# Performance work log

Measured on AMD Instinct MI355X. Metric: run time of the kernel, lower is better.

Reference implementation:

```python
import jax, jax.numpy as jnp
from jax import lax
import numpy as np

B, NG, NC = 4, 513, 512  # batch, grid size N, coef size N-1

_STENCILS = [[[-1/6, 2/3], [-1/3, -1/6]],
             [[2/3, -1/6], [-1/6, -1/3]],
             [[-1/6, -1/3], [2/3, -1/6]],
             [[-1/3, -1/6], [-1/6, 2/3]]]

def _kernel():
    # torch: vstack 4 (1,1,2,2) kernels -> permute(1,0,2,3) => (out=1, in=4, 2, 2)
    return jnp.asarray(_STENCILS, jnp.float32)[None]

def darcy(x, a, kernel):
    # x: (B,1,N,N), a: (B,1,N-1,N-1)
    N = x.shape[-1]
    X = jnp.concatenate([x[:, :, 1:N, :N-1] * a,
                         x[:, :, 1:N, 1:] * a,
                         x[:, :, :N-1, 1:] * a,
                         x[:, :, :N-1, :N-1] * a], axis=1)  # (B,4,N-1,N-1)
    Ax = lax.conv_general_dilated(X, kernel, (1, 1), 'VALID')  # (B,1,N-2,N-2)
    return jnp.pad(Ax, ((0, 0), (0, 0), (1, 1), (1, 1)))

def _conv3(x, w):
    # x: (Cin,H,W), w: (Cout,Cin,3,3), padding=1
    return lax.conv_general_dilated(x[None], w, (1, 1), ((1, 1), (1, 1)))[0]
_CONVB = jax.vmap(_conv3)

def mcc(x, w):
    # per-sample complex 3x3 conv == torch multi_channel_conv diagonal trick
    yr = _CONVB(x.real, w.real) - _CONVB(x.imag, w.imag)
    yi = _CONVB(x.real, w.imag) + _CONVB(x.imag, w.real)
    return yr + 1j * yi

def conjT(w):
    # transpose(-4,-3).transpose(-2,-1).conj()
    return jnp.conj(jnp.swapaxes(jnp.swapaxes(w, 1, 2), -2, -1))

def expand(r):
    Bb, C, M, N = r.shape
    Z = jnp.zeros((Bb, C, 2 * (M + 1), 2 * (N + 1)), r.dtype)
    Z = Z.at[:, :, 1:M+1, 1:N+1].set(r)
    Z = Z.at[:, :, M+2:, 1:N+1].set(-r[:, :, ::-1, :])
    Z = Z.at[:, :, 1:M+1, N+2:].set(-r[:, :, :, ::-1])
    Z = Z.at[:, :, M+2:, N+2:].set(r[:, :, ::-1, ::-1])
    kg = jnp.arange(-M - 1, N + 1, dtype=jnp.float32) * jnp.float32(np.pi)
    ik2 = 1.0 / (kg[:, None] ** 2 + kg[None, :] ** 2)
    ik2 = ik2.at[M + 1, N + 1].set(1.0)
    N2 = 2 * (N + 1)
    lo = N2 // 2 - N2 // 4
    hi = N2 // 2 + N2 // 4 + 1
    return Z, ik2[lo:hi, lo:hi][None, None]

def H_apply(r, w1, w2, w3, wt):
    N1 = r.shape[-1]
    rsym, ik2 = expand(r)
    N2 = rsym.shape[-1]
    lo = N2 // 2 - N2 // 4
    hi = N2 // 2 + N2 // 4 + 1
    rh = jnp.fft.fftshift(jnp.fft.ifft2(rsym, axes=(2, 3)), axes=(2, 3))[:, :, lo:hi, lo:hi]
    for w in (w1, w2, w3):
        rh = mcc(rh, w)
    out = rh * wt * ik2
    for w in (conjT(w3), conjT(w2), conjT(w1)):
        out = mcc(out, w)
    pl = N2 // 4 + 1
    pr = N2 - N2 // 2 - pl
    out = jnp.pad(out, ((0, 0), (0, 0), (pl, pr), (pl, pr)))
    e = jnp.fft.fft2(jnp.fft.ifftshift(out, axes=(2, 3)), axes=(2, 3)).real
    return e[:, :, :N1, :N1]

def fns_step(x, f, a, dinv, kernel, ws):
    # Jacobi smoother, w=3/4, M=10
    for _ in range(10):
        r = f - darcy(x, a, kernel)
        x = x.at[:, :, 1:-1, 1:-1].add(0.75 * dinv * r[:, :, 1:-1, 1:-1])
    r = f - darcy(x, a, kernel)
    e = H_apply(r[:, :, 1:-1, 1:-1], *ws)
    e = jnp.pad(e, ((0, 0), (0, 0), (1, 1), (1, 1)))
    Ae = darcy(e, a, kernel)
    alpha = (jnp.sum(r * e, axis=(1, 2, 3)) / jnp.sum(Ae * e, axis=(1, 2, 3)))[:, None, None, None]
    return x + alpha * e

def _forward(f, coef, w1, w2, w3, wt, K):
    kernel = _kernel()
    diag_k = (2.0 / 3.0) * jnp.ones((1, 1, 2, 2), jnp.float32)
    dinv = 1.0 / lax.conv_general_dilated(coef, diag_k, (1, 1), 'VALID')
    ws = (w1, w2, w3, wt)
    x = jnp.zeros_like(f)
    for _ in range(K):
        x = fns_step(x, f, coef, dinv, kernel, ws)
    r = f - darcy(x, coef, kernel)
    return jnp.linalg.norm(r.reshape(-1)) / jnp.linalg.norm(f.reshape(-1))

def setup_inputs():
    key = jax.random.key(0)
    ks = jax.random.split(key, 12)
    s = jnp.float32(0.1)
    inp = {
        'f': jax.random.normal(ks[0], (B, 1, NG, NG), jnp.float32),
        'coef': jax.random.uniform(ks[1], (B, 1, NC, NC), jnp.float32) + 0.1,
        'u': jnp.zeros((B, 1, NG, NG), jnp.float32),
        'w1r': jax.random.normal(ks[2], (B, 4, 1, 3, 3), jnp.float32) * s,
        'w1i': jax.random.normal(ks[3], (B, 4, 1, 3, 3), jnp.float32) * s,
        'w2r': jax.random.normal(ks[4], (B, 4, 4, 3, 3), jnp.float32) * s,
        'w2i': jax.random.normal(ks[5], (B, 4, 4, 3, 3), jnp.float32) * s,
        'w3r': jax.random.normal(ks[6], (B, 1, 4, 3, 3), jnp.float32) * s,
        'w3i': jax.random.normal(ks[7], (B, 1, 4, 3, 3), jnp.float32) * s,
        'wtr': jax.random.normal(ks[8], (B, 1, NG, NG), jnp.float32) * s,
        'wti': jax.random.normal(ks[9], (B, 1, NG, NG), jnp.float32) * s,
        'epoch': 101,
    }
    return inp

def reference(f, coef, u, w1r, w1i, w2r, w2i, w3r, w3i, wtr, wti, epoch):
    K = (epoch - 1) // 100 + 1
    w1 = w1r + 1j * w1i
    w2 = w2r + 1j * w2i
    w3 = w3r + 1j * w3i
    wt = wtr + 1j * wti
    return _forward(f, coef, w1, w2, w3, wt, K)
```

## Files before the change

### kernel.cpp

```cpp
#include <hip/hip_runtime.h>
#include <math.h>

#ifndef M_PI
#define M_PI 3.14159265358979323846
#endif

#define NGRID 513
#define NCELL 512
#define NINT  511
#define NB    4

constexpr int N2G = NGRID * NGRID;
constexpr int NI2 = NINT * NINT;
constexpr int NQ  = 257 * 257;

typedef unsigned short ushort;
typedef unsigned int uint32;
typedef __attribute__((ext_vector_type(8))) short short8;
typedef __attribute__((ext_vector_type(8))) unsigned short ushort8;
typedef __attribute__((ext_vector_type(4))) float f32x4;

__device__ __forceinline__ ushort f2bf(float x) {
    unsigned u = __float_as_uint(x);
    unsigned r = u + 0x7FFFu + ((u >> 16) & 1u);
    return (ushort)(r >> 16);
}
__device__ __forceinline__ float bf2f(ushort h) {
    return __uint_as_float(((unsigned)h) << 16);
}

__device__ __forceinline__ float rhq_read(const float* __restrict__ rq,
                                          int i, int j) {
    float s = 1.0f;
    if (i > 256) { i = 512 - i; s = -s; }
    if (j > 256) { j = 512 - j; s = -s; }
    return s * rq[i * 257 + j];
}

__device__ __forceinline__ float2 scale_wt(float x0, float x1, float wr, float wi,
                                           int gr, int gc) {
    int du = gr - 256, dv = gc - 256;
    float ik2;
    if (du == 0 && dv == 0)
        ik2 = 1.0f;
    else
        ik2 = (float)(1.0 / (9.869604401089358 * (double)(du * du + dv * dv)));
    return make_float2((x0 * wr - x1 * wi) * ik2, (x0 * wi + x1 * wr) * ik2);
}

__device__ __forceinline__ float darcyA(const float* __restrict__ x,
                                        const float* __restrict__ a,
                                        int i, int j) {
    const float c23 = 2.0f / 3.0f, c16 = 1.0f / 6.0f, c13 = 1.0f / 3.0f;
    float a00 = a[(i - 1) * NCELL + (j - 1)];
    float a01 = a[(i - 1) * NCELL + j];
    float a10 = a[i * NCELL + (j - 1)];
    float a11 = a[i * NCELL + j];
    const float* xm = x + (i - 1) * NGRID;
    const float* xc = x + i * NGRID;
    const float* xp = x + (i + 1) * NGRID;
    return c23 * (a00 + a01 + a10 + a11) * xc[j]
         - c16 * ((a00 + a01) * xm[j] + (a10 + a11) * xp[j]
                + (a00 + a10) * xc[j - 1] + (a01 + a11) * xc[j + 1])
         - c13 * (a00 * xm[j - 1] + a01 * xm[j + 1]
                + a10 * xp[j - 1] + a11 * xp[j + 1]);
}

__global__ void k_stencil(const float* __restrict__ xin,
                          const float* __restrict__ a,
                          const float* __restrict__ f,
                          float* __restrict__ out, int mode,
                          ushort* __restrict__ tBh, ushort* __restrict__ tBl) {
    __shared__ float st[16][17];
    int b = blockIdx.z;
    int j = blockIdx.x * 16 + threadIdx.x;
    int i = blockIdx.y * 16 + threadIdx.y;
    const float* xb = xin + (long long)b * N2G;
    const float* ab = a + (long long)b * NCELL * NCELL;
    bool ingrid = (i < NGRID && j < NGRID);
    bool interior = ingrid && i >= 1 && i <= NINT && j >= 1 && j <= NINT;
    float v = 0.0f;
    long long idx = (long long)b * N2G + (long long)i * NGRID + j;
    if (interior) {
        float Ax = darcyA(xb, ab, i, j);
        v = (mode == 0) ? f[idx] - Ax : Ax;
    } else if (ingrid) {
        v = (mode == 0) ? f[idx] : 0.0f;
    }
    if (ingrid) out[idx] = v;
    if (mode == 0 && tBh) {
        st[threadIdx.y][threadIdx.x] = v;
        __syncthreads();
        int tx = threadIdx.x, ty = threadIdx.y;
        int i2 = blockIdx.y * 16 + tx;
        int j2 = blockIdx.x * 16 + ty;
        if (i2 >= 1 && i2 <= NINT && j2 >= 1 && j2 <= NINT) {
            float rv = st[tx][ty];
            ushort h = f2bf(rv);
            long long o = (long long)b * 511 * 512
                        + (long long)(j2 - 1) * 512 + (i2 - 1);
            tBh[o] = h;
            tBl[o] = f2bf(rv - bf2f(h));
        }
    }
}

__global__ void k_jacobi5(const float* __restrict__ xin,
                          const float* __restrict__ a,
                          const float* __restrict__ f,
                          const float* __restrict__ dinv,
                          float* __restrict__ out) {
    __shared__ float sx[26][26];
    __shared__ float sa[25][26];
    __shared__ float sf[24][24];
    __shared__ float sd[24][24];
    __shared__ float sp[2][24][26];
    const float c23 = 2.0f / 3.0f, c16 = 1.0f / 6.0f, c13 = 1.0f / 3.0f;
    int b = blockIdx.z;
    const float* xb = xin + (long long)b * N2G;
    const float* ab = a + (long long)b * NCELL * NCELL;
    const float* fb = f + (long long)b * N2G;
    const float* db = dinv + (long long)b * NI2;
    int ox = blockIdx.x * 16, oy = blockIdx.y * 16;
    int tx = threadIdx.x, ty = threadIdx.y;
    int tid = ty * 16 + tx;

    for (int idx = tid; idx < 26 * 26; idx += 256) {
        int ly = idx / 26, lx = idx % 26;
        int gy = oy - 5 + ly, gx = ox - 5 + lx;
        bool in = (gy >= 0 && gy < NGRID && gx >= 0 && gx < NGRID);
        sx[ly][lx] = in ? xb[(long long)gy * NGRID + gx] : 0.0f;
    }
    for (int idx = tid; idx < 25 * 25; idx += 256) {
        int ly = idx / 25, lx = idx % 25;
        int gy = oy - 5 + ly, gx = ox - 5 + lx;
        bool in = (gy >= 0 && gy < NCELL && gx >= 0 && gx < NCELL);
        sa[ly][lx] = in ? ab[(long long)gy * NCELL + gx] : 0.0f;
    }
    for (int idx = tid; idx < 24 * 24; idx += 256) {
        int ly = idx / 24, lx = idx % 24;
        int gy = oy - 4 + ly, gx = ox - 4 + lx;
        bool ing = (gy >= 0 && gy < NGRID && gx >= 0 && gx < NGRID);
        bool itr = (gy >= 1 && gy <= NINT && gx >= 1 && gx <= NINT);
        sf[ly][lx] = ing ? fb[(long long)gy * NGRID + gx] : 0.0f;
        sd[ly][lx] = itr ? db[(long long)(gy - 1) * NINT + (gx - 1)] : 0.0f;
    }
    __syncthreads();

    for (int idx = tid; idx < 24 * 24; idx += 256) {
        int ly = idx / 24, lx = idx % 24;
        int gy = oy - 4 + ly, gx = ox - 4 + lx;
        float v = 0.0f;
        if (gy >= 0 && gy < NGRID && gx >= 0 && gx < NGRID) {
            float xc = sx[ly + 1][lx + 1];
            if (gy >= 1 && gy <= NINT && gx >= 1 && gx <= NINT) {
                float a00 = sa[ly][lx], a01 = sa[ly][lx + 1];
                float a10 = sa[ly + 1][lx], a11 = sa[ly + 1][lx + 1];
                float Ax = c23 * (a00 + a01 + a10 + a11) * xc
                    - c16 * ((a00 + a01) * sx[ly][lx + 1] + (a10 + a11) * sx[ly + 2][lx + 1]
                           + (a00 + a10) * sx[ly + 1][lx] + (a01 + a11) * sx[ly + 1][lx + 2])
                    - c13 * (a00 * sx[ly][lx] + a01 * sx[ly][lx + 2]
                           + a10 * sx[ly + 2][lx] + a11 * sx[ly + 2][lx + 2]);
                v = xc + 0.75f * sd[ly][lx] * (sf[ly][lx] - Ax);
            } else {
                v = xc;
            }
        }
        sp[0][ly][lx] = v;
    }
    __syncthreads();

    #pragma unroll 1
    for (int s = 2; s <= 4; ++s) {
        int sz = 24 - 2 * (s - 1);
        int cur = (s - 1) & 1, prv = s & 1;
        for (int idx = tid; idx < sz * sz; idx += 256) {
            int ly = idx / sz, lx = idx % sz;
            int gy = oy - (5 - s) + ly, gx = ox - (5 - s) + lx;
            float v = 0.0f;
            if (gy >= 0 && gy < NGRID && gx >= 0 && gx < NGRID) {
                float xc = sp[prv][ly + 1][lx + 1];
                if (gy >= 1 && gy <= NINT && gx >= 1 && gx <= NINT) {
                    int ar = ly + s - 1, ac = lx + s - 1;
                    float a00 = sa[ar][ac], a01 = sa[ar][ac + 1];
                    float a10 = sa[ar + 1][ac], a11 = sa[ar + 1][ac + 1];
                    float Ax = c23 * (a00 + a01 + a10 + a11) * xc
                        - c16 * ((a00 + a01) * sp[prv][ly][lx + 1] + (a10 + a11) * sp[prv][ly + 2][lx + 1]
                               + (a00 + a10) * sp[prv][ly + 1][lx] + (a01 + a11) * sp[prv][ly + 1][lx + 2])
                        - c13 * (a00 * sp[prv][ly][lx] + a01 * sp[prv][ly][lx + 2]
                               + a10 * sp[prv][ly + 2][lx] + a11 * sp[prv][ly + 2][lx + 2]);
                    int fr = ly + s - 1, fc = lx + s - 1;
                    v = xc + 0.75f * sd[fr][fc] * (sf[fr][fc] - Ax);
                } else {
                    v = xc;
                }
            }
            sp[cur][ly][lx] = v;
        }
        __syncthreads();
    }

    {
        int gy = oy + ty, gx = ox + tx;
        if (gy < NGRID && gx < NGRID) {
            float v;
            float xc = sp[1][ty + 1][tx + 1];
            if (gy >= 1 && gy <= NINT && gx >= 1 && gx <= NINT) {
                int ar = ty + 4, ac = tx + 4;
                float a00 = sa[ar][ac], a01 = sa[ar][ac + 1];
                float a10 = sa[ar + 1][ac], a11 = sa[ar + 1][ac + 1];
                float Ax = c23 * (a00 + a01 + a10 + a11) * xc
                    - c16 * ((a00 + a01) * sp[1][ty][tx + 1] + (a10 + a11) * sp[1][ty + 2][tx + 1]
                           + (a00 + a10) * sp[1][ty + 1][tx] + (a01 + a11) * sp[1][ty + 1][tx + 2])
                    - c13 * (a00 * sp[1][ty][tx] + a01 * sp[1][ty][tx + 2]
                           + a10 * sp[1][ty + 2][tx] + a11 * sp[1][ty + 2][tx + 2]);
                v = xc + 0.75f * sd[ty + 4][tx + 4] * (sf[ty + 4][tx + 4] - Ax);
            } else {
                v = xc;
            }
            out[(long long)b * N2G + (long long)gy * NGRID + gx] = v;
        }
    }
}

__global__ void k_dinv(const float* __restrict__ a, float* __restrict__ dinv) {
    long long idx = (long long)blockIdx.x * blockDim.x + threadIdx.x;
    if (idx >= (long long)NB * NI2) return;
    int b = (int)(idx / NI2);
    int rem = (int)(idx % NI2);
    int p = rem / NINT, q = rem % NINT;
    const float* ab = a + (long long)b * NCELL * NCELL;
    float s = ab[p * NCELL + q] + ab[p * NCELL + q + 1]
            + ab[(p + 1) * NCELL + q] + ab[(p + 1) * NCELL + q + 1];
    dinv[idx] = 1.0f / ((2.0f / 3.0f) * s);
}

__device__ __forceinline__ void wsplit(double v, ushort* Dh, ushort* Dl, int idx) {
    float vf = (float)v;
    ushort h = f2bf(vf);
    Dh[idx] = h;
    Dl[idx] = f2bf(vf - bf2f(h));
}

__global__ void k_genDSTA(ushort* __restrict__ Dh, ushort* __restrict__ Dl) {
    int idx = blockIdx.x * 256 + threadIdx.x;
    if (idx >= 513 * 512) return;
    int u = idx / 512, k = idx % 512;
    double v = 0.0;
    if (k < 511) {
        int t = ((u - 256) * (k + 1)) % 1024;
        if (t < 0) t += 1024;
        v = sin((M_PI / 512.0) * (double)t);
    }
    wsplit(v, Dh, Dl, idx);
}

__global__ void k_genDSTB(ushort* __restrict__ Dh, ushort* __restrict__ Dl) {
    int idx = blockIdx.x * 256 + threadIdx.x;
    if (idx >= 513 * 512) return;
    int v = idx / 512, k = idx % 512;
    double val = 0.0;
    if (k < 511) {
        int t = ((v - 256) * (k + 1)) % 1024;
        if (t < 0) t += 1024;
        val = sin((M_PI / 512.0) * (double)t) * (-1.0 / 262144.0);
    }
    wsplit(val, Dh, Dl, idx);
}

__global__ void k_genFA(ushort* __restrict__ Dh, ushort* __restrict__ Dl) {
    int idx = blockIdx.x * 256 + threadIdx.x;
    if (idx >= 511 * 1056) return;
    int y = idx / 1056, k = idx % 1056;
    double v = 0.0;
    if (k < 1026) {
        int m = (k < 513) ? k : (k - 513);
        long t = ((long)y * (m - 255)) % 1025;
        if (t < 0) t += 1025;
        double ang = (2.0 * M_PI / 1025.0) * (double)t;
        v = (k < 513) ? cos(ang) : -sin(ang);
    }
    wsplit(v, Dh, Dl, idx);
}

__global__ void k_genFB(ushort* __restrict__ Dh, ushort* __restrict__ Dl) {
    int idx = blockIdx.x * 256 + threadIdx.x;
    if (idx >= 1022 * 1056) return;
    int n = idx / 1056, k = idx % 1056;
    double v = 0.0;
    if (k < 1026) {
        int m = (k < 513) ? k : (k - 513);
        int y = (n < 511) ? n : (n - 511);
        long t = ((long)y * (m - 255)) % 1025;
        if (t < 0) t += 1025;
        double ang = (2.0 * M_PI / 1025.0) * (double)t;
        bool ktop = (k < 513), nleft = (n < 511);
        if (ktop && nleft)        v = cos(ang);
        else if (ktop && !nleft)  v = -sin(ang);
        else if (!ktop && nleft)  v = sin(ang);
        else                      v = cos(ang);
    }
    wsplit(v, Dh, Dl, idx);
}

__global__ void k_redA(const float* __restrict__ P, int nsplit, int Mr,
                       ushort* __restrict__ Dh, ushort* __restrict__ Dl) {
    int b = blockIdx.y;
    int idx = blockIdx.x * 256 + threadIdx.x;
    if (idx >= Mr * 512) return;
    int m = idx / 512, k = idx % 512;
    float v = 0.0f;
    if (k < 511) {
        long long base = (long long)m * 511 + k;
        long long str = (long long)Mr * 511;
        #pragma unroll 4
        for (int s = 0; s < nsplit; ++s)
            v += P[((long long)b * nsplit + s) * str + base];
    }
    long long o = (long long)b * Mr * 512 + idx;
    ushort h = f2bf(v);
    Dh[o] = h;
    Dl[o] = f2bf(v - bf2f(h));
}

__global__ void k_redBt(const float* __restrict__ P, int nsplit,
                        ushort* __restrict__ Dh, ushort* __restrict__ Dl) {
    int b = blockIdx.y;
    int idx = blockIdx.x * 256 + threadIdx.x;
    if (idx >= 511 * 1056) return;
    int n = idx / 1056, k = idx % 1056;
    float v = 0.0f;
    if (k < 1026) {
        int row = (k < 513) ? n : (511 + n);
        int col = (k < 513) ? k : (k - 513);
        long long base = (long long)row * 513 + col;
        float acc = 0.0f;
        #pragma unroll 4
        for (int s = 0; s < nsplit; ++s)
            acc += P[((long long)b * nsplit + s) * (1022LL * 513) + base];
        v = (k < 513) ? acc : -acc;
    }
    long long o = (long long)b * 511 * 1056 + idx;
    ushort h = f2bf(v);
    Dh[o] = h;
    Dl[o] = f2bf(v - bf2f(h));
}

__global__ __launch_bounds__(256) void k_mgemm(
    const ushort* __restrict__ Ah, const ushort* __restrict__ Al, long long bsA,
    const ushort* __restrict__ Bh, const ushort* __restrict__ Bl, long long bsB,
    float* __restrict__ C, long long bsC,
    int M, int N, int Kp, int nsplit) {
    __shared__ ushort sAh[128 * 40];
    __shared__ ushort sAl[128 * 40];
    __shared__ ushort sBh[128 * 40];
    __shared__ ushort sBl[128 * 40];

    int bz = blockIdx.z, b = bz / nsplit, ks = bz % nsplit;
    int kchunk = (((Kp + nsplit - 1) / nsplit) + 31) & ~31;
    int kbeg = ks * kchunk;
    int kend = min(Kp, kbeg + kchunk);

    Ah += b * bsA; Al += b * bsA;
    Bh += b * bsB; Bl += b * bsB;
    C += ((long long)b * nsplit + ks) * bsC;

    int bm = blockIdx.y * 128, bn = blockIdx.x * 128;
    int tid = threadIdx.x;
    int wave = tid >> 6, lane = tid & 63;
    int wm = (wave >> 1) * 64, wn = (wave & 1) * 64;
    int quad = lane >> 4, l16 = lane & 15;

    f32x4 zf = {0.f, 0.f, 0.f, 0.f};
    f32x4 acc[4][4];
    #pragma unroll
    for (int i = 0; i < 4; ++i)
        #pragma unroll
        for (int j = 0; j < 4; ++j) acc[i][j] = zf;

    int srow = tid >> 2;
    int sk8 = (tid & 3) * 8;

    for (int kt = kbeg; kt < kend; kt += 32) {
        #pragma unroll
        for (int h = 0; h < 2; ++h) {
            int row = srow + 64 * h;
            ushort8 vh = {0, 0, 0, 0, 0, 0, 0, 0};
            ushort8 vl = {0, 0, 0, 0, 0, 0, 0, 0};
            int gm = bm + row;
            if (gm < M) {
                vh = *(const ushort8*)(Ah + (long long)gm * Kp + kt + sk8);
                vl = *(const ushort8*)(Al + (long long)gm * Kp + kt + sk8);
            }
            *(ushort8*)(sAh + row * 40 + sk8) = vh;
            *(ushort8*)(sAl + row * 40 + sk8) = vl;
            ushort8 wh = {0, 0, 0, 0, 0, 0, 0, 0};
            ushort8 wl = {0, 0, 0, 0, 0, 0, 0, 0};
            int gn = bn + row;
            if (gn < N) {
                wh = *(const ushort8*)(Bh + (long long)gn * Kp + kt + sk8);
                wl = *(const ushort8*)(Bl + (long long)gn * Kp + kt + sk8);
            }
            *(ushort8*)(sBh + row * 40 + sk8) = wh;
            *(ushort8*)(sBl + row * 40 + sk8) = wl;
        }
        __syncthreads();

        short8 afh[4], afl[4], bfh[4], bfl[4];
        #pragma unroll
        for (int t = 0; t < 4; ++t) {
            int ar = wm + t * 16 + l16;
            afh[t] = *(const short8*)(sAh + ar * 40 + quad * 8);
            afl[t] = *(const short8*)(sAl + ar * 40 + quad * 8);
            int br = wn + t * 16 + l16;
            bfh[t] = *(const short8*)(sBh + br * 40 + quad * 8);
            bfl[t] = *(const short8*)(sBl + br * 40 + quad * 8);
        }
        #pragma unroll
        for (int mt = 0; mt < 4; ++mt)
            #pragma unroll
            for (int nt = 0; nt < 4; ++nt) {
                acc[mt][nt] = __builtin_amdgcn_mfma_f32_16x16x32_bf16(
                    afh[mt], bfh[nt], acc[mt][nt], 0, 0, 0);
                acc[mt][nt] = __builtin_amdgcn_mfma_f32_16x16x32_bf16(
                    afh[mt], bfl[nt], acc[mt][nt], 0, 0, 0);
                acc[mt][nt] = __builtin_amdgcn_mfma_f32_16x16x32_bf16(
                    afl[mt], bfh[nt], acc[mt][nt], 0, 0, 0);
            }
        __syncthreads();
    }

    #pragma unroll
    for (int mt = 0; mt < 4; ++mt) {
        #pragma unroll
        for (int r = 0; r < 4; ++r) {
            int gm = bm + wm + mt * 16 + quad * 4 + r;
            if (gm >= M) continue;
            long long rowoff = (long long)gm * N;
            #pragma unroll
            for (int nt = 0; nt < 4; ++nt) {
                int gn = bn + wn + nt * 16 + l16;
                if (gn < N) C[rowoff + gn] = acc[mt][nt][r];
            }
        }
    }
}

__global__ void k_reduce(const float* __restrict__ Pr,
                         float* __restrict__ outR,
                         int MN, int N, int ldo, long long bsOut, int nsplit) {
    int b = blockIdx.y;
    for (int idx = blockIdx.x * 256 + threadIdx.x; idx < MN;
         idx += gridDim.x * 256) {
        float sr = 0.0f;
        #pragma unroll 4
        for (int s = 0; s < nsplit; ++s)
            sr += Pr[((long long)b * nsplit + s) * MN + idx];
        int m = idx / N, n = idx - m * N;
        outR[(long long)b * bsOut + (long long)m * ldo + n] = sr;
    }
}

__device__ __forceinline__ float2 cmul(float2 a, float2 b) {
    return make_float2(a.x * b.x - a.y * b.y, a.x * b.y + a.y * b.x);
}

__global__ void k_compose(const float* __restrict__ w1r, const float* __restrict__ w1i,
                          const float* __restrict__ w2r, const float* __restrict__ w2i,
                          const float* __restrict__ w3r, const float* __restrict__ w3i,
                          float* __restrict__ kc) {
    int chain = blockIdx.x, b = blockIdx.y;
    int tid = threadIdx.x;
    __shared__ float2 sW1[4][9], sW2[16][9], sW3[4][9], sW21[4][25];
    for (int idx = tid; idx < 36; idx += 128) {
        int c = idx / 9, s = idx % 9, p = s / 3, q = s % 3;
        if (chain == 0) {
            int i1 = b * 36 + c * 9 + p * 3 + q;
            sW1[c][s] = make_float2(w1r[i1], w1i[i1]);
            sW3[c][s] = make_float2(w3r[i1], w3i[i1]);
        } else {
            int it = b * 36 + c * 9 + q * 3 + p;
            sW1[c][s] = make_float2(w3r[it], -w3i[it]);
            sW3[c][s] = make_float2(w1r[it], -w1i[it]);
        }
    }
    for (int idx = tid; idx < 144; idx += 128) {
        int co = idx / 36, r = idx % 36, ci = r / 9, s = r % 9, p = s / 3, q = s % 3;
        int iw = (chain == 0) ? (b * 144 + co * 36 + ci * 9 + p * 3 + q)
                              : (b * 144 + ci * 36 + co * 9 + q * 3 + p);
        float iv = w2i[iw];
        sW2[co * 4 + ci][s] = make_float2(w2r[iw], (chain == 0) ? iv : -iv);
    }
    __syncthreads();
    for (int idx = tid; idx < 100; idx += 128) {
        int cm = idx / 25, r = idx % 25, di = r / 5 - 2, dj = r % 5 - 2;
        float2 acc = make_float2(0.f, 0.f);
        for (int c1 = 0; c1 < 4; ++c1)
            for (int p = 0; p < 3; ++p)
                for (int q = 0; q < 3; ++q) {
                    int ei = di - (p - 1) + 1, ej = dj - (q - 1) + 1;
                    if (ei >= 0 && ei < 3 && ej >= 0 && ej < 3) {
                        float2 t = cmul(sW2[cm * 4 + c1][p * 3 + q], sW1[c1][ei * 3 + ej]);
                        acc.x += t.x; acc.y += t.y;
                    }
                }
        sW21[cm][r] = acc;
    }
    __syncthreads();
    for (int idx = tid; idx < 49; idx += 128) {
        int di = idx / 7 - 3, dj = idx % 7 - 3;
        float2 acc = make_float2(0.f, 0.f);
        for (int cm = 0; cm < 4; ++cm)
            for (int p = 0; p < 3; ++p)
                for (int q = 0; q < 3; ++q) {
                    int ei = di - (p - 1), ej = dj - (q - 1);
                    if (ei >= -2 && ei <= 2 && ej >= -2 && ej <= 2) {
                        float2 t = cmul(sW3[cm][p * 3 + q], sW21[cm][(ei + 2) * 5 + (ej + 2)]);
                        acc.x += t.x; acc.y += t.y;
                    }
                }
        ((float2*)kc)[(b * 2 + chain) * 49 + idx] = acc;
    }
}

template <int MODE>
__global__ __launch_bounds__(256) void k_conv7(
    const float* __restrict__ xr, const float* __restrict__ xi,
    const float* __restrict__ wtr, const float* __restrict__ wti,
    const float* __restrict__ kc,
    float* __restrict__ outr, float* __restrict__ outi,
    ushort* __restrict__ oAh, ushort* __restrict__ oAl) {
    constexpr bool CPLX = (MODE == 1);
    __shared__ float2 tile[38][23];
    __shared__ float2 kt[49];
    int b = blockIdx.z;
    int tid = threadIdx.y * 16 + threadIdx.x;
    const float2* kb = (const float2*)kc + (b * 2 + MODE) * 49;
    for (int idx = tid; idx < 49; idx += 256) kt[idx] = kb[idx];
    int row_base = blockIdx.y * 32 - 3;
    int col_base = blockIdx.x * 16 - 3;
    const float* rq = xr + (long long)b * NQ;
    for (int idx = tid; idx < 38 * 22; idx += 256) {
        int r = idx / 22, c = idx % 22;
        int gr = row_base + r, gc = col_base + c;
        float vr = 0.0f, vi = 0.0f;
        if (gr >= 0 && gr < NGRID && gc >= 0 && gc < NGRID) {
            if (MODE == 0) {
                vr = rhq_read(rq, gr, gc);
            } else {
                long long g = (long long)b * N2G + (long long)gr * NGRID + gc;
                float2 sc = scale_wt(xr[g], xi[g], wtr[g], wti[g], gr, gc);
                vr = sc.x; vi = sc.y;
            }
        }
        tile[r][c] = make_float2(vr, vi);
    }
    __syncthreads();

    int tx = threadIdx.x, r0 = threadIdx.y * 2;
    float2 acc[2];
    acc[0] = make_float2(0.f, 0.f);
    acc[1] = make_float2(0.f, 0.f);
    #pragma unroll
    for (int t = 0; t < 7; ++t) {
        float2 kv[7];
        #pragma unroll
        for (int s = 0; s < 7; ++s) kv[s] = kt[s * 7 + t];
        #pragma unroll
        for (int rr = 0; rr < 8; ++rr) {
            float2 xv = tile[r0 + rr][tx + t];
            #pragma unroll
            for (int s = 0; s < 7; ++s) {
                int orow = rr - s;
                if (orow >= 0 && orow < 2) {
                    acc[orow].x += kv[s].x * xv.x;
                    acc[orow].y += kv[s].y * xv.x;
                    if (CPLX) {
                        acc[orow].x -= kv[s].y * xv.y;
                        acc[orow].y += kv[s].x * xv.y;
                    }
                }
            }
        }
    }
    int gc = blockIdx.x * 16 + tx;
    if (gc >= NGRID) return;
    #pragma unroll
    for (int r = 0; r < 2; ++r) {
        int gr = blockIdx.y * 32 + r0 + r;
        if (gr < NGRID) {
            if (MODE == 0) {
                long long g = (long long)b * N2G + (long long)gr * NGRID + gc;
                outr[g] = acc[r].x;
                outi[g] = acc[r].y;
            } else {
                long long o = (long long)b * 513 * 1056
                            + (long long)gr * 1056 + gc;
                ushort h = f2bf(acc[r].x);
                oAh[o] = h;
                oAl[o] = f2bf(acc[r].x - bf2f(h));
                ushort h2 = f2bf(acc[r].y);
                oAh[o + 513] = h2;
                oAl[o + 513] = f2bf(acc[r].y - bf2f(h2));
            }
        }
    }
}

template <int CHAIN>
__global__ __launch_bounds__(256) void k_ring7(
    const float* __restrict__ xr, const float* __restrict__ xi,
    const float* __restrict__ wtr, const float* __restrict__ wti,
    const float* __restrict__ w1r, const float* __restrict__ w1i,
    const float* __restrict__ w2r, const float* __restrict__ w2i,
    const float* __restrict__ w3r, const float* __restrict__ w3i,
    float* __restrict__ outr, float* __restrict__ outi,
    ushort* __restrict__ oAh, ushort* __restrict__ oAl) {
    constexpr bool CPLX = (CHAIN == 1);
    __shared__ float2 W1s[4][9], W2s[16][9], W3s[4][9];
    __shared__ float2 Y[4][4][68];
    __shared__ float2 Z[4][3][66];
    int side = blockIdx.y, b = blockIdx.z;
    int u0 = blockIdx.x * 64;
    int ulo = (side < 2) ? 0 : 2;
    int uhi = (side < 2) ? (NGRID - 1) : (NGRID - 3);
    if (u0 > uhi) return;
    int tid = threadIdx.x;
    const float* rq = xr + (long long)b * NQ;

    for (int idx = tid; idx < 36; idx += 256) {
        int c = idx / 9, s = idx % 9, p = s / 3, q = s % 3;
        if (CHAIN == 0) {
            int i1 = b * 36 + c * 9 + p * 3 + q;
            W1s[c][s] = make_float2(w1r[i1], w1i[i1]);
            W3s[c][s] = make_float2(w3r[i1], w3i[i1]);
        } else {
            int it = b * 36 + c * 9 + q * 3 + p;
            W1s[c][s] = make_float2(w3r[it], -w3i[it]);
            W3s[c][s] = make_float2(w1r[it], -w1i[it]);
        }
    }
    for (int idx = tid; idx < 144; idx += 256) {
        int co = idx / 36, r = idx % 36, ci = r / 9, s = r % 9, p = s / 3, q = s % 3;
        int iw = (CHAIN == 0) ? (b * 144 + co * 36 + ci * 9 + p * 3 + q)
                              : (b * 144 + ci * 36 + co * 9 + q * 3 + p);
        float iv = w2i[iw];
        W2s[co * 4 + ci][s] = make_float2(w2r[iw], (CHAIN == 0) ? iv : -iv);
    }
    __syncthreads();

    for (int idx = tid; idx < 4 * 4 * 68; idx += 256) {
        int ch = idx / (4 * 68), r = idx % (4 * 68), d = r / 68, uu = r % 68;
        int u = u0 - 2 + uu;
        float2 acc = make_float2(0.f, 0.f);
        if (u >= 0 && u < NGRID) {
            int i, j;
            if (side == 0)      { i = d;       j = u; }
            else if (side == 1) { i = 512 - d; j = u; }
            else if (side == 2) { i = u;       j = d; }
            else                { i = u;       j = 512 - d; }
            for (int p = 0; p < 3; ++p)
                for (int q = 0; q < 3; ++q) {
                    int ii = i + p - 1, jj = j + q - 1;
                    if (ii >= 0 && ii < NGRID && jj >= 0 && jj < NGRID) {
                        float vr, vi;
                        if (CHAIN == 0) {
                            vr = rhq_read(rq, ii, jj);
                            vi = 0.0f;
                        } else {
                            long long g = (long long)b * N2G
                                        + (long long)ii * NGRID + jj;
                            float2 sc = scale_wt(xr[g], xi[g], wtr[g], wti[g],
                                                 ii, jj);
                            vr = sc.x; vi = sc.y;
                        }
                        float2 w = W1s[ch][p * 3 + q];
                        acc.x += w.x * vr - w.y * vi;
                        acc.y += w.x * vi + w.y * vr;
                    }
                }
        }
        Y[ch][d][uu] = acc;
    }
    __syncthreads();

    for (int idx = tid; idx < 4 * 3 * 66; idx += 256) {
        int co = idx / (3 * 66), r = idx % (3 * 66), d = r / 66, uu = r % 66;
        int u = u0 - 1 + uu;
        float2 acc = make_float2(0.f, 0.f);
        if (u >= 0 && u < NGRID) {
            for (int p = 0; p < 3; ++p)
                for (int q = 0; q < 3; ++q) {
                    int dd, du;
                    if (side == 0)      { dd = p - 1; du = q - 1; }
                    else if (side == 1) { dd = 1 - p; du = q - 1; }
                    else if (side == 2) { dd = q - 1; du = p - 1; }
                    else                { dd = 1 - q; du = p - 1; }
                    int d2 = d + dd, uy = uu + 1 + du;
                    if (d2 >= 0) {
                        for (int ci = 0; ci < 4; ++ci) {
                            float2 yv = Y[ci][d2][uy];
                            float2 w = W2s[co * 4 + ci][p * 3 + q];
                            acc.x += w.x * yv.x - w.y * yv.y;
                            acc.y += w.x * yv.y + w.y * yv.x;
                        }
                    }
                }
        }
        Z[co][d][uu] = acc;
    }
    __syncthreads();

    for (int idx = tid; idx < 128; idx += 256) {
        int d = idx / 64, uu = idx % 64;
        int u = u0 + uu;
        if (u < ulo || u > uhi) continue;
        float2 acc = make_float2(0.f, 0.f);
        for (int p = 0; p < 3; ++p)
            for (int q = 0; q < 3; ++q) {
                int dd, du;
                if (side == 0)      { dd = p - 1; du = q - 1; }
                else if (side == 1) { dd = 1 - p; du = q - 1; }
                else if (side == 2) { dd = q - 1; du = p - 1; }
                else                { dd = 1 - q; du = p - 1; }
                int d2 = d + dd, uz = uu + 1 + du;
                if (d2 >= 0) {
                    for (int ci = 0; ci < 4; ++ci) {
                        float2 zv = Z[ci][d2][uz];
                        float2 w = W3s[ci][p * 3 + q];
                        acc.x += w.x * zv.x - w.y * zv.y;
                        acc.y += w.x * zv.y + w.y * zv.x;
                    }
                }
            }
        int i, j;
        if (side == 0)      { i = d;       j = u; }
        else if (side == 1) { i = 512 - d; j = u; }
        else if (side == 2) { i = u;       j = d; }
        else                { i = u;       j = 512 - d; }
        if (CHAIN == 0) {
            long long g = (long long)b * N2G + (long long)i * NGRID + j;
            outr[g] = acc.x;
            outi[g] = acc.y;
        } else {
            long long o = (long long)b * 513 * 1056 + (long long)i * 1056 + j;
            ushort h = f2bf(acc.x);
            oAh[o] = h;
            oAl[o] = f2bf(acc.x - bf2f(h));
            ushort h2 = f2bf(acc.y);
            oAh[o + 513] = h2;
            oAl[o + 513] = f2bf(acc.y - bf2f(h2));
        }
    }
}

__global__ void k_dot2(const float* __restrict__ r, const float* __restrict__ e,
                       const float* __restrict__ Ae, float* __restrict__ red) {
    int b = blockIdx.y;
    const float* rb = r + (long long)b * N2G;
    const float* eb = e + (long long)b * N2G;
    const float* ab = Ae + (long long)b * N2G;
    float s1 = 0.0f, s2 = 0.0f;
    for (int i = blockIdx.x * blockDim.x + threadIdx.x; i < N2G;
         i += gridDim.x * blockDim.x) {
        float ev = eb[i];
        s1 += rb[i] * ev;
        s2 += ab[i] * ev;
    }
    #pragma unroll
    for (int o = 32; o > 0; o >>= 1) {
        s1 += __shfl_down(s1, o);
        s2 += __shfl_down(s2, o);
    }
    __shared__ float l1[4], l2[4];
    int wid = threadIdx.x >> 6;
    if ((threadIdx.x & 63) == 0) { l1[wid] = s1; l2[wid] = s2; }
    __syncthreads();
    if (threadIdx.x == 0) {
        atomicAdd(&red[2 * b], l1[0] + l1[1] + l1[2] + l1[3]);
        atomicAdd(&red[2 * b + 1], l2[0] + l2[1] + l2[2] + l2[3]);
    }
}

__global__ void k_update(float* __restrict__ x, const float* __restrict__ e,
                         const float* __restrict__ red) {
    long long idx = (long long)blockIdx.x * blockDim.x + threadIdx.x;
    if (idx >= (long long)NB * N2G) return;
    int b = (int)(idx / N2G);
    float alpha = red[2 * b] / red[2 * b + 1];
    x[idx] += alpha * e[idx];
}

__global__ void k_norm(const float* __restrict__ r, const float* __restrict__ f,
                       float* __restrict__ red) {
    float s1 = 0.0f, s2 = 0.0f;
    for (long long i = (long long)blockIdx.x * blockDim.x + threadIdx.x;
         i < (long long)NB * N2G; i += (long long)gridDim.x * blockDim.x) {
        float rv = r[i], fv = f[i];
        s1 += rv * rv;
        s2 += fv * fv;
    }
    #pragma unroll
    for (int o = 32; o > 0; o >>= 1) {
        s1 += __shfl_down(s1, o);
        s2 += __shfl_down(s2, o);
    }
    __shared__ float l1[4], l2[4];
    int wid = threadIdx.x >> 6;
    if ((threadIdx.x & 63) == 0) { l1[wid] = s1; l2[wid] = s2; }
    __syncthreads();
    if (threadIdx.x == 0) {
        atomicAdd(&red[8], l1[0] + l1[1] + l1[2] + l1[3]);
        atomicAdd(&red[9], l2[0] + l2[1] + l2[2] + l2[3]);
    }
}

__global__ void k_final(const float* __restrict__ red, float* __restrict__ out) {
    out[0] = sqrtf(red[8] / red[9]);
}

extern "C" void kernel_launch(void* const* d_in, const int* in_sizes, int n_in,
                              void* d_out, int out_size, void* d_ws, size_t ws_size,
                              hipStream_t stream) {
    (void)in_sizes; (void)n_in; (void)out_size; (void)ws_size;
    const float* f    = (const float*)d_in[0];
    const float* coef = (const float*)d_in[1];
    const float* w1r  = (const float*)d_in[3];
    const float* w1i  = (const float*)d_in[4];
    const float* w2r  = (const float*)d_in[5];
    const float* w2i  = (const float*)d_in[6];
    const float* w3r  = (const float*)d_in[7];
    const float* w3i  = (const float*)d_in[8];
    const float* wtr  = (const float*)d_in[9];
    const float* wti  = (const float*)d_in[10];
    float* out = (float*)d_out;

    float* ws = (float*)d_ws;
    size_t off = 0;
    auto alloc = [&](long long n) {
        float* p = ws + off;
        off += (size_t)((n + 3) & ~3LL);
        return p;
    };
    float* x0   = alloc((long long)NB * N2G);
    float* x1   = alloc((long long)NB * N2G);
    float* rr   = alloc((long long)NB * N2G);
    float* ee   = alloc((long long)NB * N2G);
    float* dinv = alloc((long long)NB * NI2);
    float* c1r  = alloc((long long)NB * 4 * N2G);
    float* c1i  = alloc((long long)NB * 4 * N2G);
    float* c2r  = alloc((long long)NB * 4 * N2G);
    float* c2i  = alloc((long long)NB * 4 * N2G);
    float* pr   = c1r;
    float* or_  = alloc((long long)NB * N2G);
    float* oi_  = alloc((long long)NB * N2G);
    float* rhq  = alloc((long long)NB * NQ);
    float* red  = alloc(16);
    ushort* sGh  = (ushort*)alloc(513 * 512 / 2);
    ushort* sGl  = (ushort*)alloc(513 * 512 / 2);
    ushort* sGth = (ushort*)alloc(513 * 512 / 2);
    ushort* sGtl = (ushort*)alloc(513 * 512 / 2);
    ushort* sFAh = (ushort*)alloc(511 * 1056 / 2);
    ushort* sFAl = (ushort*)alloc(511 * 1056 / 2);
    ushort* sFBh = (ushort*)alloc(1022 * 1056 / 2);
    ushort* sFBl = (ushort*)alloc(1022 * 1056 / 2);
    ushort* dA2h = (ushort*)alloc((long long)NB * 257 * 512 / 2);
    ushort* dA2l = (ushort*)alloc((long long)NB * 257 * 512 / 2);
    ushort* dA3h = (ushort*)alloc((long long)NB * 513 * 1056 / 2);
    ushort* dA3l = (ushort*)alloc((long long)NB * 513 * 1056 / 2);
    ushort* dB1h = (ushort*)alloc((long long)NB * 511 * 512 / 2);
    ushort* dB1l = (ushort*)alloc((long long)NB * 511 * 512 / 2);
    ushort* dB4h = (ushort*)alloc((long long)NB * 511 * 1056 / 2);
    ushort* dB4l = (ushort*)alloc((long long)NB * 511 * 1056 / 2);
    float* kcomp = alloc(NB * 2 * 49 * 2);
    float* Ae   = or_;

    dim3 blk2(16, 16);
    dim3 grdS(33, 33, NB);
    dim3 grdC(33, 17, NB);
    dim3 grdR(9, 4, NB);
    const int SP = 4;

    hipMemsetAsync(x0, 0, (size_t)NB * N2G * sizeof(float), stream);
    hipMemsetAsync(dA3h, 0, (size_t)NB * 513 * 1056 * 2 * 2, stream);
    hipMemsetAsync(dB1h, 0, (size_t)NB * 511 * 512 * 2 * 2, stream);
    k_dinv<<<dim3((NB * NI2 + 255) / 256), dim3(256), 0, stream>>>(coef, dinv);
    k_genDSTA<<<dim3((513 * 512 + 255) / 256), dim3(256), 0, stream>>>(sGh, sGl);
    k_genDSTB<<<dim3((513 * 512 + 255) / 256), dim3(256), 0, stream>>>(sGth, sGtl);
    k_genFA<<<dim3((511 * 1056 + 255) / 256), dim3(256), 0, stream>>>(sFAh, sFAl);
    k_genFB<<<dim3((1022 * 1056 + 255) / 256), dim3(256), 0, stream>>>(sFBh, sFBl);
    k_compose<<<dim3(2, NB), dim3(128), 0, stream>>>(w1r, w1i, w2r, w2i, w3r, w3i, kcomp);

    float* xa = x0;
    float* xb = x1;
    for (int step = 0; step < 2; ++step) {
        for (int it = 0; it < 2; ++it) {
            k_jacobi5<<<grdS, blk2, 0, stream>>>(xa, coef, f, dinv, xb);
            float* t = xa; xa = xb; xb = t;
        }
        k_stencil<<<grdS, blk2, 0, stream>>>(xa, coef, f, rr, 0, dB1h, dB1l);

        k_mgemm<<<dim3(4, 3, NB * SP), dim3(256), 0, stream>>>(
            sGh, sGl, 0, dB1h, dB1l, (long long)511 * 512,
            pr, (long long)257 * 511, 257, 511, 512, SP);
        k_redA<<<dim3((257 * 512 + 255) / 256, NB), dim3(256), 0, stream>>>(
            pr, SP, 257, dA2h, dA2l);
        k_mgemm<<<dim3(3, 3, NB * SP), dim3(256), 0, stream>>>(
            dA2h, dA2l, (long long)257 * 512, sGth, sGtl, 0,
            pr, (long long)NQ, 257, 257, 512, SP);
        k_reduce<<<dim3(259, NB), dim3(256), 0, stream>>>(
            pr, rhq, NQ, 257, 257, (long long)NQ, SP);

        k_conv7<0><<<grdC, blk2, 0, stream>>>(
            rhq, nullptr, nullptr, nullptr, kcomp, or_, oi_, nullptr, nullptr);
        k_ring7<0><<<grdR, dim3(256), 0, stream>>>(
            rhq, nullptr, nullptr, nullptr,
            w1r, w1i, w2r, w2i, w3r, w3i, or_, oi_, nullptr, nullptr);
        k_conv7<1><<<grdC, blk2, 0, stream>>>(
            or_, oi_, wtr, wti, kcomp, nullptr, nullptr, dA3h, dA3l);
        k_ring7<1><<<grdR, dim3(256), 0, stream>>>(
            or_, oi_, wtr, wti,
            w1r, w1i, w2r, w2i, w3r, w3i, nullptr, nullptr, dA3h, dA3l);

        k_mgemm<<<dim3(5, 8, NB * 4), dim3(256), 0, stream>>>(
            sFBh, sFBl, 0, dA3h, dA3l, (long long)513 * 1056,
            pr, 1022LL * 513, 1022, 513, 1056, 4);
        k_redBt<<<dim3(2109, NB), dim3(256), 0, stream>>>(pr, 4, dB4h, dB4l);
        k_mgemm<<<dim3(4, 4, NB * SP), dim3(256), 0, stream>>>(
            sFAh, sFAl, 0, dB4h, dB4l, (long long)511 * 1056,
            pr, (long long)NI2, 511, 511, 1056, SP);
        hipMemsetAsync(ee, 0, (size_t)NB * N2G * sizeof(float), stream);
        k_reduce<<<dim3(1024, NB), dim3(256), 0, stream>>>(
            pr, ee + NGRID + 1, NI2, NINT, NGRID, (long long)N2G, SP);

        k_stencil<<<grdS, blk2, 0, stream>>>(ee, coef, nullptr, Ae, 2,
                                             nullptr, nullptr);
        hipMemsetAsync(red, 0, 8 * sizeof(float), stream);
        k_dot2<<<dim3(64, NB), dim3(256), 0, stream>>>(rr, ee, Ae, red);
        k_update<<<dim3((NB * N2G + 255) / 256), dim3(256), 0, stream>>>(xa, ee, red);
    }
    k_stencil<<<grdS, blk2, 0, stream>>>(xa, coef, f, rr, 0, nullptr, nullptr);
    hipMemsetAsync(red + 8, 0, 2 * sizeof(float), stream);
    k_norm<<<dim3(256), dim3(256), 0, stream>>>(rr, f, red);
    k_final<<<dim3(1), dim3(1), 0, stream>>>(red, out);
}
```

Before: 683.1 us.

## Fuse Jacobi smoothing with residual, Ae into dot, and final update into norm

```diff
diff --git a/kernel.cpp b/kernel.cpp
--- a/kernel.cpp
+++ b/kernel.cpp
@@ -66,55 +66,22 @@
                 + a10 * xp[j - 1] + a11 * xp[j + 1]);
 }
 
-__global__ void k_stencil(const float* __restrict__ xin,
-                          const float* __restrict__ a,
-                          const float* __restrict__ f,
-                          float* __restrict__ out, int mode,
-                          ushort* __restrict__ tBh, ushort* __restrict__ tBl) {
+template <int RES>
+__global__ __launch_bounds__(256) void k_jacobi5R(
+    const float* __restrict__ xin, const float* __restrict__ a,
+    const float* __restrict__ f, const float* __restrict__ dinv,
+    float* __restrict__ out, float* __restrict__ rout,
+    ushort* __restrict__ tBh, ushort* __restrict__ tBl) {
+    constexpr int H  = RES ? 6 : 5;
+    constexpr int SX = 16 + 2 * H;
+    constexpr int SA = SX - 1;
+    constexpr int SF = 16 + 2 * (H - 1);
+    __shared__ float sx[SX][SX];
+    __shared__ float sa[SA][SA + 1];
+    __shared__ float sf[SF][SF];
+    __shared__ float sd[SF][SF];
+    __shared__ float sp[2][SF][SF + 2];
     __shared__ float st[16][17];
-    int b = blockIdx.z;
-    int j = blockIdx.x * 16 + threadIdx.x;
-    int i = blockIdx.y * 16 + threadIdx.y;
-    const float* xb = xin + (long long)b * N2G;
-    const float* ab = a + (long long)b * NCELL * NCELL;
-    bool ingrid = (i < NGRID && j < NGRID);
-    bool interior = ingrid && i >= 1 && i <= NINT && j >= 1 && j <= NINT;
-    float v = 0.0f;
-    long long idx = (long long)b * N2G + (long long)i * NGRID + j;
-    if (interior) {
-        float Ax = darcyA(xb, ab, i, j);
-        v = (mode == 0) ? f[idx] - Ax : Ax;
-    } else if (ingrid) {
-        v = (mode == 0) ? f[idx] : 0.0f;
-    }
-    if (ingrid) out[idx] = v;
-    if (mode == 0 && tBh) {
-        st[threadIdx.y][threadIdx.x] = v;
-        __syncthreads();
-        int tx = threadIdx.x, ty = threadIdx.y;
-        int i2 = blockIdx.y * 16 + tx;
-        int j2 = blockIdx.x * 16 + ty;
-        if (i2 >= 1 && i2 <= NINT && j2 >= 1 && j2 <= NINT) {
-            float rv = st[tx][ty];
-            ushort h = f2bf(rv);
-            long long o = (long long)b * 511 * 512
-                        + (long long)(j2 - 1) * 512 + (i2 - 1);
-            tBh[o] = h;
-            tBl[o] = f2bf(rv - bf2f(h));
-        }
-    }
-}
-
-__global__ void k_jacobi5(const float* __restrict__ xin,
-                          const float* __restrict__ a,
-                          const float* __restrict__ f,
-                          const float* __restrict__ dinv,
-                          float* __restrict__ out) {
-    __shared__ float sx[26][26];
-    __shared__ float sa[25][26];
-    __shared__ float sf[24][24];
-    __shared__ float sd[24][24];
-    __shared__ float sp[2][24][26];
     const float c23 = 2.0f / 3.0f, c16 = 1.0f / 6.0f, c13 = 1.0f / 3.0f;
     int b = blockIdx.z;
     const float* xb = xin + (long long)b * N2G;
@@ -125,21 +92,21 @@
     int tx = threadIdx.x, ty = threadIdx.y;
     int tid = ty * 16 + tx;
 
-    for (int idx = tid; idx < 26 * 26; idx += 256) {
-        int ly = idx / 26, lx = idx % 26;
-        int gy = oy - 5 + ly, gx = ox - 5 + lx;
+    for (int idx = tid; idx < SX * SX; idx += 256) {
+        int ly = idx / SX, lx = idx % SX;
+        int gy = oy - H + ly, gx = ox - H + lx;
         bool in = (gy >= 0 && gy < NGRID && gx >= 0 && gx < NGRID);
         sx[ly][lx] = in ? xb[(long long)gy * NGRID + gx] : 0.0f;
     }
-    for (int idx = tid; idx < 25 * 25; idx += 256) {
-        int ly = idx / 25, lx = idx % 25;
-        int gy = oy - 5 + ly, gx = ox - 5 + lx;
+    for (int idx = tid; idx < SA * SA; idx += 256) {
+        int ly = idx / SA, lx = idx % SA;
+        int gy = oy - H + ly, gx = ox - H + lx;
         bool in = (gy >= 0 && gy < NCELL && gx >= 0 && gx < NCELL);
         sa[ly][lx] = in ? ab[(long long)gy * NCELL + gx] : 0.0f;
     }
-    for (int idx = tid; idx < 24 * 24; idx += 256) {
-        int ly = idx / 24, lx = idx % 24;
-        int gy = oy - 4 + ly, gx = ox - 4 + lx;
+    for (int idx = tid; idx < SF * SF; idx += 256) {
+        int ly = idx / SF, lx = idx % SF;
+        int gy = oy - (H - 1) + ly, gx = ox - (H - 1) + lx;
         bool ing = (gy >= 0 && gy < NGRID && gx >= 0 && gx < NGRID);
         bool itr = (gy >= 1 && gy <= NINT && gx >= 1 && gx <= NINT);
         sf[ly][lx] = ing ? fb[(long long)gy * NGRID + gx] : 0.0f;
@@ -147,9 +114,9 @@
     }
     __syncthreads();
 
-    for (int idx = tid; idx < 24 * 24; idx += 256) {
-        int ly = idx / 24, lx = idx % 24;
-        int gy = oy - 4 + ly, gx = ox - 4 + lx;
+    for (int idx = tid; idx < SF * SF; idx += 256) {
+        int ly = idx / SF, lx = idx % SF;
+        int gy = oy - (H - 1) + ly, gx = ox - (H - 1) + lx;
         float v = 0.0f;
         if (gy >= 0 && gy < NGRID && gx >= 0 && gx < NGRID) {
             float xc = sx[ly + 1][lx + 1];
@@ -171,12 +138,12 @@
     __syncthreads();
 
     #pragma unroll 1
-    for (int s = 2; s <= 4; ++s) {
-        int sz = 24 - 2 * (s - 1);
+    for (int s = 2; s <= 5; ++s) {
+        int sz = 16 + 2 * (H - s);
         int cur = (s - 1) & 1, prv = s & 1;
         for (int idx = tid; idx < sz * sz; idx += 256) {
             int ly = idx / sz, lx = idx % sz;
-            int gy = oy - (5 - s) + ly, gx = ox - (5 - s) + lx;
+            int gy = oy - (H - s) + ly, gx = ox - (H - s) + lx;
             float v = 0.0f;
             if (gy >= 0 && gy < NGRID && gx >= 0 && gx < NGRID) {
                 float xc = sp[prv][ly + 1][lx + 1];
@@ -200,25 +167,40 @@
         __syncthreads();
     }
 
-    {
-        int gy = oy + ty, gx = ox + tx;
+    int gy = oy + ty, gx = ox + tx;
+    long long gidx = (long long)b * N2G + (long long)gy * NGRID + gx;
+    if constexpr (!RES) {
+        if (gy < NGRID && gx < NGRID) out[gidx] = sp[0][ty][tx];
+    } else {
+        float rv = 0.0f;
         if (gy < NGRID && gx < NGRID) {
-            float v;
-            float xc = sp[1][ty + 1][tx + 1];
+            float x5 = sp[0][ty + 1][tx + 1];
+            out[gidx] = x5;
             if (gy >= 1 && gy <= NINT && gx >= 1 && gx <= NINT) {
-                int ar = ty + 4, ac = tx + 4;
-                float a00 = sa[ar][ac], a01 = sa[ar][ac + 1];
-                float a10 = sa[ar + 1][ac], a11 = sa[ar + 1][ac + 1];
-                float Ax = c23 * (a00 + a01 + a10 + a11) * xc
-                    - c16 * ((a00 + a01) * sp[1][ty][tx + 1] + (a10 + a11) * sp[1][ty + 2][tx + 1]
-                           + (a00 + a10) * sp[1][ty + 1][tx] + (a01 + a11) * sp[1][ty + 1][tx + 2])
-                    - c13 * (a00 * sp[1][ty][tx] + a01 * sp[1][ty][tx + 2]
-                           + a10 * sp[1][ty + 2][tx] + a11 * sp[1][ty + 2][tx + 2]);
-                v = xc + 0.75f * sd[ty + 4][tx + 4] * (sf[ty + 4][tx + 4] - Ax);
+                float a00 = sa[ty + 5][tx + 5], a01 = sa[ty + 5][tx + 6];
+                float a10 = sa[ty + 6][tx + 5], a11 = sa[ty + 6][tx + 6];
+                float Ax = c23 * (a00 + a01 + a10 + a11) * x5
+                    - c16 * ((a00 + a01) * sp[0][ty][tx + 1] + (a10 + a11) * sp[0][ty + 2][tx + 1]
+                           + (a00 + a10) * sp[0][ty + 1][tx] + (a01 + a11) * sp[0][ty + 1][tx + 2])
+                    - c13 * (a00 * sp[0][ty][tx] + a01 * sp[0][ty][tx + 2]
+                           + a10 * sp[0][ty + 2][tx] + a11 * sp[0][ty + 2][tx + 2]);
+                rv = sf[ty + 5][tx + 5] - Ax;
             } else {
-                v = xc;
-            }
-            out[(long long)b * N2G + (long long)gy * NGRID + gx] = v;
+                rv = sf[ty + 5][tx + 5];
+            }
+            rout[gidx] = rv;
+        }
+        st[ty][tx] = rv;
+        __syncthreads();
+        int i2 = blockIdx.y * 16 + tx;
+        int j2 = blockIdx.x * 16 + ty;
+        if (i2 >= 1 && i2 <= NINT && j2 >= 1 && j2 <= NINT) {
+            float r2 = st[tx][ty];
+            ushort h = f2bf(r2);
+            long long o = (long long)b * 511 * 512
+                        + (long long)(j2 - 1) * 512 + (i2 - 1);
+            tBh[o] = h;
+            tBl[o] = f2bf(r2 - bf2f(h));
         }
     }
 }
@@ -754,18 +736,21 @@
     }
 }
 
-__global__ void k_dot2(const float* __restrict__ r, const float* __restrict__ e,
-                       const float* __restrict__ Ae, float* __restrict__ red) {
+__global__ void k_dotAe(const float* __restrict__ r, const float* __restrict__ e,
+                        const float* __restrict__ a, float* __restrict__ red) {
     int b = blockIdx.y;
     const float* rb = r + (long long)b * N2G;
     const float* eb = e + (long long)b * N2G;
-    const float* ab = Ae + (long long)b * N2G;
+    const float* ab = a + (long long)b * NCELL * NCELL;
     float s1 = 0.0f, s2 = 0.0f;
-    for (int i = blockIdx.x * blockDim.x + threadIdx.x; i < N2G;
-         i += gridDim.x * blockDim.x) {
-        float ev = eb[i];
-        s1 += rb[i] * ev;
-        s2 += ab[i] * ev;
+    for (int idx = blockIdx.x * blockDim.x + threadIdx.x; idx < NI2;
+         idx += gridDim.x * blockDim.x) {
+        int i = idx / NINT + 1, j = idx % NINT + 1;
+        long long g = (long long)i * NGRID + j;
+        float ev = eb[g];
+        float Ax = darcyA(eb, ab, i, j);
+        s1 += rb[g] * ev;
+        s2 += Ax * ev;
     }
     #pragma unroll
     for (int o = 32; o > 0; o >>= 1) {
@@ -791,12 +776,43 @@
     x[idx] += alpha * e[idx];
 }
 
-__global__ void k_norm(const float* __restrict__ r, const float* __restrict__ f,
-                       float* __restrict__ red) {
+__global__ void k_fin(const float* __restrict__ x, const float* __restrict__ e,
+                      const float* __restrict__ f, const float* __restrict__ a,
+                      float* __restrict__ red) {
+    const float c23 = 2.0f / 3.0f, c16 = 1.0f / 6.0f, c13 = 1.0f / 3.0f;
+    int b = blockIdx.y;
+    long long base = (long long)b * N2G;
+    const float* ab = a + (long long)b * NCELL * NCELL;
+    float alpha = red[8 + 2 * b] / red[8 + 2 * b + 1];
     float s1 = 0.0f, s2 = 0.0f;
-    for (long long i = (long long)blockIdx.x * blockDim.x + threadIdx.x;
-         i < (long long)NB * N2G; i += (long long)gridDim.x * blockDim.x) {
-        float rv = r[i], fv = f[i];
+    for (int idx = blockIdx.x * blockDim.x + threadIdx.x; idx < N2G;
+         idx += gridDim.x * blockDim.x) {
+        int i = idx / NGRID, j = idx - i * NGRID;
+        float fv = f[base + idx];
+        float rv = fv;
+        if (i >= 1 && i <= NINT && j >= 1 && j <= NINT) {
+            float a00 = ab[(i - 1) * NCELL + (j - 1)];
+            float a01 = ab[(i - 1) * NCELL + j];
+            float a10 = ab[i * NCELL + (j - 1)];
+            float a11 = ab[i * NCELL + j];
+            long long gm = base + (long long)(i - 1) * NGRID + j;
+            long long gc = base + (long long)i * NGRID + j;
+            long long gp = base + (long long)(i + 1) * NGRID + j;
+            float xmm = x[gm - 1] + alpha * e[gm - 1];
+            float xm0 = x[gm] + alpha * e[gm];
+            float xmp = x[gm + 1] + alpha * e[gm + 1];
+            float xcm = x[gc - 1] + alpha * e[gc - 1];
+            float xc0 = x[gc] + alpha * e[gc];
+            float xcp = x[gc + 1] + alpha * e[gc + 1];
+            float xpm = x[gp - 1] + alpha * e[gp - 1];
+            float xp0 = x[gp] + alpha * e[gp];
+            float xpp = x[gp + 1] + alpha * e[gp + 1];
+            float Ax = c23 * (a00 + a01 + a10 + a11) * xc0
+                - c16 * ((a00 + a01) * xm0 + (a10 + a11) * xp0
+                       + (a00 + a10) * xcm + (a01 + a11) * xcp)
+                - c13 * (a00 * xmm + a01 * xmp + a10 * xpm + a11 * xpp);
+            rv = fv - Ax;
+        }
         s1 += rv * rv;
         s2 += fv * fv;
     }
@@ -810,13 +826,13 @@
     if ((threadIdx.x & 63) == 0) { l1[wid] = s1; l2[wid] = s2; }
     __syncthreads();
     if (threadIdx.x == 0) {
-        atomicAdd(&red[8], l1[0] + l1[1] + l1[2] + l1[3]);
-        atomicAdd(&red[9], l2[0] + l2[1] + l2[2] + l2[3]);
+        atomicAdd(&red[16], l1[0] + l1[1] + l1[2] + l1[3]);
+        atomicAdd(&red[17], l2[0] + l2[1] + l2[2] + l2[3]);
     }
 }
 
 __global__ void k_final(const float* __restrict__ red, float* __restrict__ out) {
-    out[0] = sqrtf(red[8] / red[9]);
+    out[0] = sqrtf(red[16] / red[17]);
 }
 
 extern "C" void kernel_launch(void* const* d_in, const int* in_sizes, int n_in,
@@ -855,7 +871,7 @@
     float* or_  = alloc((long long)NB * N2G);
     float* oi_  = alloc((long long)NB * N2G);
     float* rhq  = alloc((long long)NB * NQ);
-    float* red  = alloc(16);
+    float* red  = alloc(20);
     ushort* sGh  = (ushort*)alloc(513 * 512 / 2);
     ushort* sGl  = (ushort*)alloc(513 * 512 / 2);
     ushort* sGth = (ushort*)alloc(513 * 512 / 2);
@@ -873,7 +889,6 @@
     ushort* dB4h = (ushort*)alloc((long long)NB * 511 * 1056 / 2);
     ushort* dB4l = (ushort*)alloc((long long)NB * 511 * 1056 / 2);
     float* kcomp = alloc(NB * 2 * 49 * 2);
-    float* Ae   = or_;
 
     dim3 blk2(16, 16);
     dim3 grdS(33, 33, NB);
@@ -882,6 +897,8 @@
     const int SP = 4;
 
     hipMemsetAsync(x0, 0, (size_t)NB * N2G * sizeof(float), stream);
+    hipMemsetAsync(ee, 0, (size_t)NB * N2G * sizeof(float), stream);
+    hipMemsetAsync(red, 0, 20 * sizeof(float), stream);
     hipMemsetAsync(dA3h, 0, (size_t)NB * 513 * 1056 * 2 * 2, stream);
     hipMemsetAsync(dB1h, 0, (size_t)NB * 511 * 512 * 2 * 2, stream);
     k_dinv<<<dim3((NB * NI2 + 255) / 256), dim3(256), 0, stream>>>(coef, dinv);
@@ -891,14 +908,11 @@
     k_genFB<<<dim3((1022 * 1056 + 255) / 256), dim3(256), 0, stream>>>(sFBh, sFBl);
     k_compose<<<dim3(2, NB), dim3(128), 0, stream>>>(w1r, w1i, w2r, w2i, w3r, w3i, kcomp);
 
-    float* xa = x0;
-    float* xb = x1;
     for (int step = 0; step < 2; ++step) {
-        for (int it = 0; it < 2; ++it) {
-            k_jacobi5<<<grdS, blk2, 0, stream>>>(xa, coef, f, dinv, xb);
-            float* t = xa; xa = xb; xb = t;
-        }
-        k_stencil<<<grdS, blk2, 0, stream>>>(xa, coef, f, rr, 0, dB1h, dB1l);
+        k_jacobi5R<0><<<grdS, blk2, 0, stream>>>(
+            x0, coef, f, dinv, x1, nullptr, nullptr, nullptr);
+        k_jacobi5R<1><<<grdS, blk2, 0, stream>>>(
+            x1, coef, f, dinv, x0, rr, dB1h, dB1l);
 
         k_mgemm<<<dim3(4, 3, NB * SP), dim3(256), 0, stream>>>(
             sGh, sGl, 0, dB1h, dB1l, (long long)511 * 512,
@@ -929,18 +943,15 @@
         k_mgemm<<<dim3(4, 4, NB * SP), dim3(256), 0, stream>>>(
             sFAh, sFAl, 0, dB4h, dB4l, (long long)511 * 1056,
             pr, (long long)NI2, 511, 511, 1056, SP);
-        hipMemsetAsync(ee, 0, (size_t)NB * N2G * sizeof(float), stream);
         k_reduce<<<dim3(1024, NB), dim3(256), 0, stream>>>(
             pr, ee + NGRID + 1, NI2, NINT, NGRID, (long long)N2G, SP);
 
-        k_stencil<<<grdS, blk2, 0, stream>>>(ee, coef, nullptr, Ae, 2,
-                                             nullptr, nullptr);
-        hipMemsetAsync(red, 0, 8 * sizeof(float), stream);
-        k_dot2<<<dim3(64, NB), dim3(256), 0, stream>>>(rr, ee, Ae, red);
-        k_update<<<dim3((NB * N2G + 255) / 256), dim3(256), 0, stream>>>(xa, ee, red);
-    }
-    k_stencil<<<grdS, blk2, 0, stream>>>(xa, coef, f, rr, 0, nullptr, nullptr);
-    hipMemsetAsync(red + 8, 0, 2 * sizeof(float), stream);
-    k_norm<<<dim3(256), dim3(256), 0, stream>>>(rr, f, red);
+        k_dotAe<<<dim3(128, NB), dim3(256), 0, stream>>>(
+            rr, ee, coef, red + 8 * step);
+        if (step == 0)
+            k_update<<<dim3((NB * N2G + 255) / 256), dim3(256), 0, stream>>>(
+                x0, ee, red);
+    }
+    k_fin<<<dim3(128, NB), dim3(256), 0, stream>>>(x0, ee, f, coef, red);
     k_final<<<dim3(1), dim3(1), 0, stream>>>(red, out);
 }
```

After: 683.8 us. No clear change (+0.1%).
